# Performance work log

Hardware: AMD Instinct MI355X
Metric: run time of the kernel (lower is better)

## Reference

```python
import jax, jax.numpy as jnp
import numpy as np

B, D, K = 65536, 256, 10
LOG_2PI = float(np.log(2.0 * np.pi))


def setup_inputs() -> dict:
    key = jax.random.key(0)
    k1, k2 = jax.random.split(key)
    q_z = jax.random.normal(k1, (B, D), dtype=jnp.float32)
    # Xavier-uniform init for mu lookup (approximated with normal scale)
    mu_table = jax.random.normal(k2, (K, D), dtype=jnp.float32) * 0.1
    # logvar lookup initialized to log(exp(0)**2) = 0
    logvar_table = jnp.zeros((K, D), dtype=jnp.float32)
    return {"q_z": q_z, "mu_table": mu_table, "logvar_table": logvar_table}


def reference(q_z, mu_table, logvar_table):
    # q_z: [B, D]; mu_table, logvar_table: [K, D]
    k = mu_table.shape[0]
    diff = q_z[:, None, :] - mu_table[None, :, :]              # [B, K, D]
    llh = -0.5 * (diff * diff / jnp.exp(logvar_table)[None]
                  + logvar_table[None] + LOG_2PI)              # [B, K, D]
    log_q_y_logit = jnp.sum(llh, axis=2) + jnp.log(1.0 / k)    # [B, K]
    q_y = jax.nn.softmax(log_q_y_logit, axis=1)                # [B, K]
    ind = jnp.argmax(q_y, axis=1)                              # [B]
    return (log_q_y_logit, q_y, ind)
```

## Files before the change

kernel.cpp:

```cpp
#include <hip/hip_runtime.h>
#include <hip/hip_bf16.h>
#include <math.h>

#define BB 65536
#define DD 256
#define KK 10
#define LOG_2PI 1.8378770664093453f

__global__ __launch_bounds__(DD) void gmvae_prep(
    const float* __restrict__ mu_table,
    const float* __restrict__ logvar_table,
    float* __restrict__ tab,
    float* __restrict__ C)
{
    const int k = blockIdx.x;
    const int d = threadIdx.x;
    const float lv = logvar_table[k * DD + d];
    const float m  = mu_table[k * DD + d];
    const float iv = expf(-lv);
    const float a  = m * iv;

    const int f    = d >> 2;
    const int s    = f >> 4;
    const int c    = (f >> 2) & 3;
    const int jj   = f & 3;
    const int comp = d & 3;
    const int idx_f4 = ((s * 4 + jj) * KK + k) * 2;
    const int base   = c * 1280 + idx_f4 * 4 + comp;
    tab[base]     = iv;
    tab[base + 4] = -2.0f * a;

    float p = fmaf(m, a, lv);
    __shared__ float red[4];
    #pragma unroll
    for (int off = 32; off > 0; off >>= 1)
        p += __shfl_down(p, off, 64);
    if ((threadIdx.x & 63) == 0)
        red[threadIdx.x >> 6] = p;
    __syncthreads();
    if (threadIdx.x == 0) {
        const float s2 = (red[0] + red[1]) + (red[2] + red[3]);
        C[k] = -0.5f * (s2 + 256.0f * LOG_2PI) + logf(0.1f);
    }
}

__device__ __forceinline__ float rl(float v, int lane) {
    return __int_as_float(__builtin_amdgcn_readlane(__float_as_int(v), lane));
}

__global__ __launch_bounds__(256) void gmvae_main(
    const float* __restrict__ q_z,
    const float* __restrict__ tab,
    const float* __restrict__ C,
    float* __restrict__ out)
{
    __shared__ float4 buf[2 * 64 * 17];
    float* comb = reinterpret_cast<float*>(buf);

    const int t    = threadIdx.x;
    const int r    = t & 63;
    const int c    = __builtin_amdgcn_readfirstlane(t >> 6);
    const int row0 = blockIdx.x * 64;

    const float4* __restrict__ q4 = reinterpret_cast<const float4*>(q_z);

    const float4* __restrict__ t4 =
        reinterpret_cast<const float4*>(tab) + c * 320;
    float4 w[5];
    #pragma unroll
    for (int i = 0; i < 5; ++i)
        w[i] = t4[i * 64 + r];

    const int rr0 = t >> 4;
    const int ff  = t & 15;

    float acc[KK];
    #pragma unroll
    for (int k = 0; k < KK; ++k) acc[k] = 0.f;

    float4 v[4];
    #pragma unroll
    for (int i = 0; i < 4; ++i)
        v[i] = q4[(size_t)(row0 + i * 16 + rr0) * 64 + 0 * 16 + ff];
    #pragma unroll
    for (int i = 0; i < 4; ++i)
        buf[(i * 16 + rr0) * 17 + ff] = v[i];
    __syncthreads();

    #pragma unroll
    for (int s = 0; s < 4; ++s) {
        if (s < 3) {
            #pragma unroll
            for (int i = 0; i < 4; ++i)
                v[i] = q4[(size_t)(row0 + i * 16 + rr0) * 64 + (s + 1) * 16 + ff];
        }

        const float4* bp = buf + (s & 1) * (64 * 17) + r * 17 + c * 4;
        #pragma unroll
        for (int jj = 0; jj < 4; ++jj) {
            const float4 q = bp[jj];
            const float qx2 = q.x * q.x, qy2 = q.y * q.y;
            const float qz2 = q.z * q.z, qw2 = q.w * q.w;
            #pragma unroll
            for (int k = 0; k < KK; ++k) {
                const int flat = ((s * 4 + jj) * KK + k) * 2;
                const int i = flat >> 6;
                const int L = flat & 63;
                const float4 wv = w[i];
                acc[k] = fmaf(qx2, rl(wv.x, L),     acc[k]);
                acc[k] = fmaf(q.x, rl(wv.x, L + 1), acc[k]);
                acc[k] = fmaf(qy2, rl(wv.y, L),     acc[k]);
                acc[k] = fmaf(q.y, rl(wv.y, L + 1), acc[k]);
                acc[k] = fmaf(qz2, rl(wv.z, L),     acc[k]);
                acc[k] = fmaf(q.z, rl(wv.z, L + 1), acc[k]);
                acc[k] = fmaf(qw2, rl(wv.w, L),     acc[k]);
                acc[k] = fmaf(q.w, rl(wv.w, L + 1), acc[k]);
            }
        }

        if (s < 3) {
            float4* wp = buf + ((s + 1) & 1) * (64 * 17);
            #pragma unroll
            for (int i = 0; i < 4; ++i)
                wp[(i * 16 + rr0) * 17 + ff] = v[i];
            __syncthreads();
        }
    }

    __syncthreads();
    #pragma unroll
    for (int k = 0; k < KK; ++k)
        comb[t * 11 + k] = acc[k];
    __syncthreads();

    if (t < 64) {
        float l[KK];
        #pragma unroll
        for (int k = 0; k < KK; ++k) {
            const float vsum =
                ((comb[r * 11 + k]         + comb[(64 + r) * 11 + k]) +
                 (comb[(128 + r) * 11 + k] + comb[(192 + r) * 11 + k]));
            l[k] = fmaf(vsum, -0.5f, C[k]);
        }

        float mx = l[0];
        #pragma unroll
        for (int k = 1; k < KK; ++k) mx = fmaxf(mx, l[k]);

        float e[KK];
        float sum = 0.f;
        #pragma unroll
        for (int k = 0; k < KK; ++k) { e[k] = __expf(l[k] - mx); sum += e[k]; }
        const float inv = 1.0f / sum;

        int idx = 0;
        float best = l[0];
        #pragma unroll
        for (int k = 1; k < KK; ++k)
            if (l[k] > best) { best = l[k]; idx = k; }

        const int row = row0 + r;
        float2* __restrict__ o1 =
            reinterpret_cast<float2*>(out) + (size_t)row * 5;
        float2* __restrict__ o2 =
            reinterpret_cast<float2*>(out + (size_t)BB * KK) + (size_t)row * 5;
        #pragma unroll
        for (int k = 0; k < 5; ++k)
            o1[k] = make_float2(l[2 * k], l[2 * k + 1]);
        #pragma unroll
        for (int k = 0; k < 5; ++k)
            o2[k] = make_float2(e[2 * k] * inv, e[2 * k + 1] * inv);
        out[(size_t)2 * BB * KK + row] = (float)idx;
    }
}

extern "C" void kernel_launch(void* const* d_in, const int* in_sizes, int n_in,
                              void* d_out, int out_size, void* d_ws, size_t ws_size,
                              hipStream_t stream) {
    const float* q_z    = (const float*)d_in[0];
    const float* mu     = (const float*)d_in[1];
    const float* logvar = (const float*)d_in[2];
    float* out = (float*)d_out;

    float* tab = (float*)d_ws;
    float* C   = tab + 5120;

    gmvae_prep<<<KK, DD, 0, stream>>>(mu, logvar, tab, C);
    gmvae_main<<<BB / 64, 256, 0, stream>>>(q_z, tab, C, out);
}
```

Measured before the change: 104.1 us.

## Fuse table-prep kernel into main kernel, recomputing per block

Removes the separate prep kernel and has every block compute its inverse-variance and mean-scaled weights and the per-cluster constants directly from mu and logvar tables. This drops one kernel launch and the workspace round trip, and the first q_z loads are issued before the table work to overlap latency. The cost is redundant exp and reduction work in all 1024 blocks plus extra small table loads, and launch bounds now request 4 blocks per CU.

```diff
diff --git a/kernel.cpp b/kernel.cpp
--- a/kernel.cpp
+++ b/kernel.cpp
@@ -1,5 +1,4 @@
 #include <hip/hip_runtime.h>
-#include <hip/hip_bf16.h>
 #include <math.h>
 
 #define BB 65536
@@ -7,54 +6,19 @@
 #define KK 10
 #define LOG_2PI 1.8378770664093453f
 
-__global__ __launch_bounds__(DD) void gmvae_prep(
-    const float* __restrict__ mu_table,
-    const float* __restrict__ logvar_table,
-    float* __restrict__ tab,
-    float* __restrict__ C)
-{
-    const int k = blockIdx.x;
-    const int d = threadIdx.x;
-    const float lv = logvar_table[k * DD + d];
-    const float m  = mu_table[k * DD + d];
-    const float iv = expf(-lv);
-    const float a  = m * iv;
-
-    const int f    = d >> 2;
-    const int s    = f >> 4;
-    const int c    = (f >> 2) & 3;
-    const int jj   = f & 3;
-    const int comp = d & 3;
-    const int idx_f4 = ((s * 4 + jj) * KK + k) * 2;
-    const int base   = c * 1280 + idx_f4 * 4 + comp;
-    tab[base]     = iv;
-    tab[base + 4] = -2.0f * a;
-
-    float p = fmaf(m, a, lv);
-    __shared__ float red[4];
-    #pragma unroll
-    for (int off = 32; off > 0; off >>= 1)
-        p += __shfl_down(p, off, 64);
-    if ((threadIdx.x & 63) == 0)
-        red[threadIdx.x >> 6] = p;
-    __syncthreads();
-    if (threadIdx.x == 0) {
-        const float s2 = (red[0] + red[1]) + (red[2] + red[3]);
-        C[k] = -0.5f * (s2 + 256.0f * LOG_2PI) + logf(0.1f);
-    }
-}
-
 __device__ __forceinline__ float rl(float v, int lane) {
     return __int_as_float(__builtin_amdgcn_readlane(__float_as_int(v), lane));
 }
 
-__global__ __launch_bounds__(256) void gmvae_main(
+__global__ __launch_bounds__(256, 4) void gmvae_fused(
     const float* __restrict__ q_z,
-    const float* __restrict__ tab,
-    const float* __restrict__ C,
+    const float* __restrict__ mu_table,
+    const float* __restrict__ logvar_table,
     float* __restrict__ out)
 {
     __shared__ float4 buf[2 * 64 * 17];
+    __shared__ float red[KK * 4];
+    __shared__ float Cs[KK];
     float* comb = reinterpret_cast<float*>(buf);
 
     const int t    = threadIdx.x;
@@ -64,24 +28,61 @@
 
     const float4* __restrict__ q4 = reinterpret_cast<const float4*>(q_z);
 
-    const float4* __restrict__ t4 =
-        reinterpret_cast<const float4*>(tab) + c * 320;
+    const int rr0 = t >> 4;
+    const int ff  = t & 15;
+
+    float4 v[4];
+    #pragma unroll
+    for (int i = 0; i < 4; ++i)
+        v[i] = q4[(size_t)(row0 + i * 16 + rr0) * 64 + 0 * 16 + ff];
+
+    const float4* __restrict__ mu4 = reinterpret_cast<const float4*>(mu_table);
+    const float4* __restrict__ lv4 = reinterpret_cast<const float4*>(logvar_table);
+    const int odd = r & 1;
     float4 w[5];
     #pragma unroll
-    for (int i = 0; i < 5; ++i)
-        w[i] = t4[i * 64 + r];
+    for (int i = 0; i < 5; ++i) {
+        const int qq = i * 32 + (r >> 1);
+        const int k  = qq % KK;
+        const int sj = qq / KK;
+        const int f  = (sj >> 2) * 16 + c * 4 + (sj & 3);
+        const float4 lv = lv4[k * 64 + f];
+        const float4 m  = mu4[k * 64 + f];
+        const float iv0 = expf(-lv.x), iv1 = expf(-lv.y);
+        const float iv2 = expf(-lv.z), iv3 = expf(-lv.w);
+        if (odd) {
+            const float a0 = m.x * iv0, a1 = m.y * iv1;
+            const float a2 = m.z * iv2, a3 = m.w * iv3;
+            w[i] = make_float4(-2.0f * a0, -2.0f * a1, -2.0f * a2, -2.0f * a3);
+        } else {
+            w[i] = make_float4(iv0, iv1, iv2, iv3);
+        }
+    }
 
-    const int rr0 = t >> 4;
-    const int ff  = t & 15;
+    #pragma unroll
+    for (int k = 0; k < KK; ++k) {
+        const float lvv = logvar_table[k * DD + t];
+        const float m   = mu_table[k * DD + t];
+        const float iv  = expf(-lvv);
+        const float a   = m * iv;
+        float p = fmaf(m, a, lvv);
+        #pragma unroll
+        for (int off = 32; off > 0; off >>= 1)
+            p += __shfl_down(p, off, 64);
+        if (r == 0)
+            red[k * 4 + c] = p;
+    }
+    __syncthreads();
+    if (t < KK) {
+        const float s2 = (red[t * 4 + 0] + red[t * 4 + 1]) +
+                         (red[t * 4 + 2] + red[t * 4 + 3]);
+        Cs[t] = -0.5f * (s2 + 256.0f * LOG_2PI) + logf(0.1f);
+    }
 
     float acc[KK];
     #pragma unroll
     for (int k = 0; k < KK; ++k) acc[k] = 0.f;
 
-    float4 v[4];
-    #pragma unroll
-    for (int i = 0; i < 4; ++i)
-        v[i] = q4[(size_t)(row0 + i * 16 + rr0) * 64 + 0 * 16 + ff];
     #pragma unroll
     for (int i = 0; i < 4; ++i)
         buf[(i * 16 + rr0) * 17 + ff] = v[i];
@@ -140,7 +141,7 @@
             const float vsum =
                 ((comb[r * 11 + k]         + comb[(64 + r) * 11 + k]) +
                  (comb[(128 + r) * 11 + k] + comb[(192 + r) * 11 + k]));
-            l[k] = fmaf(vsum, -0.5f, C[k]);
+            l[k] = fmaf(vsum, -0.5f, Cs[k]);
         }
 
         float mx = l[0];
@@ -180,11 +181,6 @@
     const float* q_z    = (const float*)d_in[0];
     const float* mu     = (const float*)d_in[1];
     const float* logvar = (const float*)d_in[2];
-    float* out = (float*)d_out;
-
-    float* tab = (float*)d_ws;
-    float* C   = tab + 5120;
-
-    gmvae_prep<<<KK, DD, 0, stream>>>(mu, logvar, tab, C);
-    gmvae_main<<<BB / 64, 256, 0, stream>>>(q_z, tab, C, out);
+    (void)d_ws; (void)ws_size;
+    gmvae_fused<<<BB / 64, 256, 0, stream>>>(q_z, mu, logvar, (float*)d_out);
 }
```

Result: slower. 119.2 us (+14.5%).

## Process two rows per thread so each readlane broadcast feeds twice the FMAs

Applied to the files above, without the earlier changes.

Each block now handles 128 rows instead of 64. Every thread keeps two accumulator sets and reuses each readlane-broadcast table value for two rows, which halves the broadcast overhead per FMA and halves the number of blocks. The lookup table and constants also move from the workspace pointer into device globals. The cost is more registers and twice the LDS per block (about 70 KB), which can lower occupancy, and the epilogue reduction is done by 128 threads.

```diff
diff --git a/kernel.cpp b/kernel.cpp
--- a/kernel.cpp
+++ b/kernel.cpp
@@ -1,5 +1,4 @@
 #include <hip/hip_runtime.h>
-#include <hip/hip_bf16.h>
 #include <math.h>
 
 #define BB 65536
@@ -7,12 +6,14 @@
 #define KK 10
 #define LOG_2PI 1.8378770664093453f
 
+__device__ float4 g_tab4[1280];
+__device__ float  g_C[KK];
+
 __global__ __launch_bounds__(DD) void gmvae_prep(
     const float* __restrict__ mu_table,
-    const float* __restrict__ logvar_table,
-    float* __restrict__ tab,
-    float* __restrict__ C)
+    const float* __restrict__ logvar_table)
 {
+    float* tab = reinterpret_cast<float*>(g_tab4);
     const int k = blockIdx.x;
     const int d = threadIdx.x;
     const float lv = logvar_table[k * DD + d];
@@ -40,7 +41,7 @@
     __syncthreads();
     if (threadIdx.x == 0) {
         const float s2 = (red[0] + red[1]) + (red[2] + red[3]);
-        C[k] = -0.5f * (s2 + 256.0f * LOG_2PI) + logf(0.1f);
+        g_C[k] = -0.5f * (s2 + 256.0f * LOG_2PI) + logf(0.1f);
     }
 }
 
@@ -50,40 +51,38 @@
 
 __global__ __launch_bounds__(256) void gmvae_main(
     const float* __restrict__ q_z,
-    const float* __restrict__ tab,
-    const float* __restrict__ C,
     float* __restrict__ out)
 {
-    __shared__ float4 buf[2 * 64 * 17];
+    __shared__ float4 buf[2 * 128 * 17];
     float* comb = reinterpret_cast<float*>(buf);
 
     const int t    = threadIdx.x;
     const int r    = t & 63;
     const int c    = __builtin_amdgcn_readfirstlane(t >> 6);
-    const int row0 = blockIdx.x * 64;
+    const int row0 = blockIdx.x * 128;
 
     const float4* __restrict__ q4 = reinterpret_cast<const float4*>(q_z);
 
-    const float4* __restrict__ t4 =
-        reinterpret_cast<const float4*>(tab) + c * 320;
+    const int rr0 = t >> 4;
+    const int ff  = t & 15;
+
+    float4 v[8];
+    #pragma unroll
+    for (int i = 0; i < 8; ++i)
+        v[i] = q4[(size_t)(row0 + i * 16 + rr0) * 64 + 0 * 16 + ff];
+
+    const float4* __restrict__ t4 = g_tab4 + c * 320;
     float4 w[5];
     #pragma unroll
     for (int i = 0; i < 5; ++i)
         w[i] = t4[i * 64 + r];
 
-    const int rr0 = t >> 4;
-    const int ff  = t & 15;
-
-    float acc[KK];
-    #pragma unroll
-    for (int k = 0; k < KK; ++k) acc[k] = 0.f;
-
-    float4 v[4];
-    #pragma unroll
-    for (int i = 0; i < 4; ++i)
-        v[i] = q4[(size_t)(row0 + i * 16 + rr0) * 64 + 0 * 16 + ff];
-    #pragma unroll
-    for (int i = 0; i < 4; ++i)
+    float accA[KK], accB[KK];
+    #pragma unroll
+    for (int k = 0; k < KK; ++k) { accA[k] = 0.f; accB[k] = 0.f; }
+
+    #pragma unroll
+    for (int i = 0; i < 8; ++i)
         buf[(i * 16 + rr0) * 17 + ff] = v[i];
     __syncthreads();
 
@@ -91,37 +90,53 @@
     for (int s = 0; s < 4; ++s) {
         if (s < 3) {
             #pragma unroll
-            for (int i = 0; i < 4; ++i)
+            for (int i = 0; i < 8; ++i)
                 v[i] = q4[(size_t)(row0 + i * 16 + rr0) * 64 + (s + 1) * 16 + ff];
         }
 
-        const float4* bp = buf + (s & 1) * (64 * 17) + r * 17 + c * 4;
+        const float4* bpA = buf + (s & 1) * (128 * 17) + r * 17 + c * 4;
+        const float4* bpB = bpA + 64 * 17;
         #pragma unroll
         for (int jj = 0; jj < 4; ++jj) {
-            const float4 q = bp[jj];
-            const float qx2 = q.x * q.x, qy2 = q.y * q.y;
-            const float qz2 = q.z * q.z, qw2 = q.w * q.w;
+            const float4 qa = bpA[jj];
+            const float4 qb = bpB[jj];
+            const float ax2 = qa.x * qa.x, ay2 = qa.y * qa.y;
+            const float az2 = qa.z * qa.z, aw2 = qa.w * qa.w;
+            const float bx2 = qb.x * qb.x, by2 = qb.y * qb.y;
+            const float bz2 = qb.z * qb.z, bw2 = qb.w * qb.w;
             #pragma unroll
             for (int k = 0; k < KK; ++k) {
                 const int flat = ((s * 4 + jj) * KK + k) * 2;
                 const int i = flat >> 6;
                 const int L = flat & 63;
                 const float4 wv = w[i];
-                acc[k] = fmaf(qx2, rl(wv.x, L),     acc[k]);
-                acc[k] = fmaf(q.x, rl(wv.x, L + 1), acc[k]);
-                acc[k] = fmaf(qy2, rl(wv.y, L),     acc[k]);
-                acc[k] = fmaf(q.y, rl(wv.y, L + 1), acc[k]);
-                acc[k] = fmaf(qz2, rl(wv.z, L),     acc[k]);
-                acc[k] = fmaf(q.z, rl(wv.z, L + 1), acc[k]);
-                acc[k] = fmaf(qw2, rl(wv.w, L),     acc[k]);
-                acc[k] = fmaf(q.w, rl(wv.w, L + 1), acc[k]);
+                const float ivx = rl(wv.x, L), nax = rl(wv.x, L + 1);
+                const float ivy = rl(wv.y, L), nay = rl(wv.y, L + 1);
+                const float ivz = rl(wv.z, L), naz = rl(wv.z, L + 1);
+                const float ivw = rl(wv.w, L), naw = rl(wv.w, L + 1);
+                accA[k] = fmaf(ax2, ivx, accA[k]);
+                accA[k] = fmaf(qa.x, nax, accA[k]);
+                accA[k] = fmaf(ay2, ivy, accA[k]);
+                accA[k] = fmaf(qa.y, nay, accA[k]);
+                accA[k] = fmaf(az2, ivz, accA[k]);
+                accA[k] = fmaf(qa.z, naz, accA[k]);
+                accA[k] = fmaf(aw2, ivw, accA[k]);
+                accA[k] = fmaf(qa.w, naw, accA[k]);
+                accB[k] = fmaf(bx2, ivx, accB[k]);
+                accB[k] = fmaf(qb.x, nax, accB[k]);
+                accB[k] = fmaf(by2, ivy, accB[k]);
+                accB[k] = fmaf(qb.y, nay, accB[k]);
+                accB[k] = fmaf(bz2, ivz, accB[k]);
+                accB[k] = fmaf(qb.z, naz, accB[k]);
+                accB[k] = fmaf(bw2, ivw, accB[k]);
+                accB[k] = fmaf(qb.w, naw, accB[k]);
             }
         }
 
         if (s < 3) {
-            float4* wp = buf + ((s + 1) & 1) * (64 * 17);
+            float4* wp = buf + ((s + 1) & 1) * (128 * 17);
             #pragma unroll
-            for (int i = 0; i < 4; ++i)
+            for (int i = 0; i < 8; ++i)
                 wp[(i * 16 + rr0) * 17 + ff] = v[i];
             __syncthreads();
         }
@@ -129,18 +144,23 @@
 
     __syncthreads();
     #pragma unroll
-    for (int k = 0; k < KK; ++k)
-        comb[t * 11 + k] = acc[k];
-    __syncthreads();
-
-    if (t < 64) {
+    for (int k = 0; k < KK; ++k) {
+        comb[t * 11 + k]         = accA[k];
+        comb[(256 + t) * 11 + k] = accB[k];
+    }
+    __syncthreads();
+
+    if (t < 128) {
+        const int hb = t >> 6;
+        const int rr = t & 63;
+        const int cb = hb * 256 + rr;
         float l[KK];
         #pragma unroll
         for (int k = 0; k < KK; ++k) {
             const float vsum =
-                ((comb[r * 11 + k]         + comb[(64 + r) * 11 + k]) +
-                 (comb[(128 + r) * 11 + k] + comb[(192 + r) * 11 + k]));
-            l[k] = fmaf(vsum, -0.5f, C[k]);
+                ((comb[cb * 11 + k]         + comb[(cb + 64) * 11 + k]) +
+                 (comb[(cb + 128) * 11 + k] + comb[(cb + 192) * 11 + k]));
+            l[k] = fmaf(vsum, -0.5f, g_C[k]);
         }
 
         float mx = l[0];
@@ -159,7 +179,7 @@
         for (int k = 1; k < KK; ++k)
             if (l[k] > best) { best = l[k]; idx = k; }
 
-        const int row = row0 + r;
+        const int row = row0 + t;
         float2* __restrict__ o1 =
             reinterpret_cast<float2*>(out) + (size_t)row * 5;
         float2* __restrict__ o2 =
@@ -180,11 +200,7 @@
     const float* q_z    = (const float*)d_in[0];
     const float* mu     = (const float*)d_in[1];
     const float* logvar = (const float*)d_in[2];
-    float* out = (float*)d_out;
-
-    float* tab = (float*)d_ws;
-    float* C   = tab + 5120;
-
-    gmvae_prep<<<KK, DD, 0, stream>>>(mu, logvar, tab, C);
-    gmvae_main<<<BB / 64, 256, 0, stream>>>(q_z, tab, C, out);
-}
+    (void)d_ws; (void)ws_size;
+    gmvae_prep<<<KK, DD, 0, stream>>>(mu, logvar);
+    gmvae_main<<<BB / 128, 256, 0, stream>>>(q_z, (float*)d_out);
+}
```

New measurement: 101.7 us (median of 2 runs). 1.02x faster.
